# Kernel tuning notes

Hardware: AMD Instinct MI355X
Metric: run time of the kernel (lower is better)

Reference implementation:

```python
import jax, jax.numpy as jnp
import numpy as np

B, L, H = 16, 512, 1024
HEADS, HEAD_SIZE = 12, 64
NEG = 1e12


def sinusoidal_position_embedding(seq_len, output_dim):
    pos = jnp.arange(seq_len, dtype=jnp.float32)[:, None]
    idx = jnp.arange(output_dim // 2, dtype=jnp.float32)
    freqs = pos * jnp.power(10000.0, -2.0 * idx / output_dim)  # [L, D/2]
    emb = jnp.stack([jnp.sin(freqs), jnp.cos(freqs)], axis=-1)  # [L, D/2, 2]
    return emb.reshape(seq_len, output_dim)  # interleaved sin/cos, [L, D]


def setup_inputs() -> dict:
    key = jax.random.key(0)
    k1, k2, k3 = jax.random.split(key, 3)
    inputs = jax.random.normal(k1, (B, L, H), dtype=jnp.float32)
    mask = jnp.ones((B, L), dtype=jnp.int32)
    W = jax.random.normal(k2, (H, HEADS * HEAD_SIZE * 2), dtype=jnp.float32) / np.sqrt(H)
    b = jax.random.normal(k3, (HEADS * HEAD_SIZE * 2,), dtype=jnp.float32) * 0.01
    pos_emb = sinusoidal_position_embedding(L, HEAD_SIZE)  # [L, HEAD_SIZE]
    return {"inputs": inputs, "mask": mask, "W": W, "b": b, "pos_emb": pos_emb}


def rotate_half_interleaved(x):
    # stack([-x[..., 1::2], x[..., ::2]], -1).reshape(x.shape)
    x2 = jnp.stack([-x[..., 1::2], x[..., ::2]], axis=-1)
    return x2.reshape(x.shape)


def reference(inputs, mask, W, b, pos_emb):
    bsz, seq_len, _ = inputs.shape
    d = pos_emb.shape[-1]
    heads = W.shape[1] // (2 * d)
    out = inputs @ W + b                       # [B, L, heads*2d]
    out = out.reshape(bsz, seq_len, heads, 2 * d)
    qw, kw = out[..., :d], out[..., d:]        # [B, L, heads, d]
    cos_pos = jnp.repeat(pos_emb[:, 1::2], 2, axis=-1)[None, :, None, :]  # [1,L,1,d]
    sin_pos = jnp.repeat(pos_emb[:, 0::2], 2, axis=-1)[None, :, None, :]
    qw = qw * cos_pos + rotate_half_interleaved(qw) * sin_pos
    kw = kw * cos_pos + rotate_half_interleaved(kw) * sin_pos
    logits = jnp.einsum('bmhd,bnhd->bhmn', qw, kw)  # [B, heads, L, L]
    pad = mask.astype(logits.dtype)[:, None, None, :] * mask.astype(logits.dtype)[:, None, :, None]
    # torch code: expand of mask[:,None,None,:] -> applies along last axis only;
    # replicate exactly: pad_mask broadcasts mask over the query axis.
    pad_mask = jnp.broadcast_to(mask.astype(logits.dtype)[:, None, None, :], logits.shape)
    logits = logits * pad_mask - (1.0 - pad_mask) * NEG
    tril = jnp.tril(jnp.ones((seq_len, seq_len), dtype=logits.dtype), -1)
    logits = logits - tril[None, None, :, :] * NEG
    return logits / jnp.sqrt(jnp.array(d, dtype=logits.dtype))
```

## Files before the change

kernel.cpp:

```cpp
#include <hip/hip_runtime.h>

#define BB 16
#define LL 512
#define HH 1024
#define HEADS 12
#define DD 64
#define N1 1536
#define M1 8192
#define NEGC 1e12f

typedef short bf16x8 __attribute__((ext_vector_type(8)));
typedef float f32x4 __attribute__((ext_vector_type(4)));

__device__ __forceinline__ unsigned short f2bf(float f) {
    union { float f; unsigned int u; } v; v.f = f;
    unsigned int u = v.u;
    return (unsigned short)((u + 0x7fffu + ((u >> 16) & 1u)) >> 16);
}

__global__ __launch_bounds__(256) void k_conv_x(const float* __restrict__ X,
                                                unsigned short* __restrict__ Xb,
                                                int n4) {
    int i = blockIdx.x * 256 + threadIdx.x;
    if (i >= n4) return;
    float4 v = ((const float4*)X)[i];
    ushort4 o;
    o.x = f2bf(v.x); o.y = f2bf(v.y); o.z = f2bf(v.z); o.w = f2bf(v.w);
    ((ushort4*)Xb)[i] = o;
}

__global__ __launch_bounds__(256) void k_trans_w(const float* __restrict__ W,
                                                 unsigned short* __restrict__ Wt) {
    __shared__ float tile[32][33];
    int n0 = blockIdx.x * 32;
    int k0 = blockIdx.y * 32;
    int tx = threadIdx.x;
    int ty = threadIdx.y;
#pragma unroll
    for (int i = 0; i < 4; i++) {
        int k = ty + i * 8;
        tile[k][tx] = W[(size_t)(k0 + k) * N1 + n0 + tx];
    }
    __syncthreads();
#pragma unroll
    for (int i = 0; i < 4; i++) {
        int n = ty + i * 8;
        Wt[(size_t)(n0 + n) * HH + k0 + tx] = f2bf(tile[tx][n]);
    }
}

__global__ __launch_bounds__(256) void k_gemm1_rope(
    const unsigned short* __restrict__ Xb,
    const unsigned short* __restrict__ Wt,
    const float* __restrict__ bias,
    const float* __restrict__ pe,
    unsigned short* __restrict__ Qr,
    unsigned short* __restrict__ Kr)
{
    __shared__ __align__(16) unsigned short As[64 * 40];
    __shared__ __align__(16) unsigned short Bs[64 * 40];
    int m0 = blockIdx.y * 64;
    int n0 = blockIdx.x * 64;
    int tid = threadIdx.x;
    int w  = tid >> 6;
    int ln = tid & 63;
    int lq = ln >> 4;
    int lm = ln & 15;
    int mw = (w & 1) * 32;
    int nw = (w >> 1) * 32;

    int srow = tid >> 2;
    int scol = (tid & 3) * 8;

    f32x4 acc[2][2] = {};

    for (int kk = 0; kk < HH; kk += 32) {
        uint4 av = *(const uint4*)&Xb[(size_t)(m0 + srow) * HH + kk + scol];
        uint4 bv = *(const uint4*)&Wt[(size_t)(n0 + srow) * HH + kk + scol];
        *(uint4*)&As[srow * 40 + scol] = av;
        *(uint4*)&Bs[srow * 40 + scol] = bv;
        __syncthreads();
        bf16x8 af0 = *(const bf16x8*)&As[(mw + lm) * 40 + lq * 8];
        bf16x8 af1 = *(const bf16x8*)&As[(mw + 16 + lm) * 40 + lq * 8];
        bf16x8 bf0 = *(const bf16x8*)&Bs[(nw + lm) * 40 + lq * 8];
        bf16x8 bf1 = *(const bf16x8*)&Bs[(nw + 16 + lm) * 40 + lq * 8];
        acc[0][0] = __builtin_amdgcn_mfma_f32_16x16x32_bf16(af0, bf0, acc[0][0], 0, 0, 0);
        acc[0][1] = __builtin_amdgcn_mfma_f32_16x16x32_bf16(af0, bf1, acc[0][1], 0, 0, 0);
        acc[1][0] = __builtin_amdgcn_mfma_f32_16x16x32_bf16(af1, bf0, acc[1][0], 0, 0, 0);
        acc[1][1] = __builtin_amdgcn_mfma_f32_16x16x32_bf16(af1, bf1, acc[1][1], 0, 0, 0);
        __syncthreads();
    }

#pragma unroll
    for (int nt = 0; nt < 2; nt++) {
        int n = n0 + nw + nt * 16 + lm;
        float bv = bias[n];
        int h = n >> 7;
        int c = n & 127;
        int j = c & 63;
        int ii = j >> 1;
        bool isK = (c >= 64);
#pragma unroll
        for (int mt = 0; mt < 2; mt++) {
#pragma unroll
            for (int r = 0; r < 4; r++) {
                int m = m0 + mw + mt * 16 + lq * 4 + r;
                int l = m & (LL - 1);
                int bidx = m >> 9;
                float v = acc[mt][nt][r] + bv;
                float vp = __shfl_xor(v, 1, 64);
                float sv = pe[l * 64 + 2 * ii];
                float cv = pe[l * 64 + 2 * ii + 1];
                float o = (j & 1) ? (v * cv + vp * sv) : (v * cv - vp * sv);
                unsigned short ob = f2bf(o);
                size_t idx = ((size_t)(bidx * HEADS + h) * LL + l) * DD + j;
                if (isK) Kr[idx] = ob; else Qr[idx] = ob;
            }
        }
    }
}

__global__ __launch_bounds__(256) void k_gemm2(
    const unsigned short* __restrict__ Qr,
    const unsigned short* __restrict__ Kr,
    const int* __restrict__ mask,
    float* __restrict__ out)
{
    __shared__ __align__(16) unsigned short Qs[64 * 72];
    __shared__ __align__(16) unsigned short Ks[64 * 72];
    int bh = blockIdx.z;
    int b  = bh / HEADS;
    int n0 = blockIdx.x * 64;
    int m0 = blockIdx.y * 64;
    int tid = threadIdx.x;
    int w  = tid >> 6;
    int ln = tid & 63;
    int lq = ln >> 4;
    int lm = ln & 15;
    int mw = (w & 1) * 32;
    int nw = (w >> 1) * 32;

    const unsigned short* Qb = Qr + (size_t)bh * LL * DD;
    const unsigned short* Kb = Kr + (size_t)bh * LL * DD;

    int srow = tid >> 3;
    int scol = (tid & 7) * 8;
#pragma unroll
    for (int p = 0; p < 2; p++) {
        int row = srow + p * 32;
        *(uint4*)&Qs[row * 72 + scol] = *(const uint4*)&Qb[(size_t)(m0 + row) * DD + scol];
        *(uint4*)&Ks[row * 72 + scol] = *(const uint4*)&Kb[(size_t)(n0 + row) * DD + scol];
    }
    __syncthreads();

    f32x4 acc[2][2] = {};
#pragma unroll
    for (int kk = 0; kk < 64; kk += 32) {
        bf16x8 a0 = *(const bf16x8*)&Qs[(mw + lm) * 72 + kk + lq * 8];
        bf16x8 a1 = *(const bf16x8*)&Qs[(mw + 16 + lm) * 72 + kk + lq * 8];
        bf16x8 b0 = *(const bf16x8*)&Ks[(nw + lm) * 72 + kk + lq * 8];
        bf16x8 b1 = *(const bf16x8*)&Ks[(nw + 16 + lm) * 72 + kk + lq * 8];
        acc[0][0] = __builtin_amdgcn_mfma_f32_16x16x32_bf16(a0, b0, acc[0][0], 0, 0, 0);
        acc[0][1] = __builtin_amdgcn_mfma_f32_16x16x32_bf16(a0, b1, acc[0][1], 0, 0, 0);
        acc[1][0] = __builtin_amdgcn_mfma_f32_16x16x32_bf16(a1, b0, acc[1][0], 0, 0, 0);
        acc[1][1] = __builtin_amdgcn_mfma_f32_16x16x32_bf16(a1, b1, acc[1][1], 0, 0, 0);
    }

#pragma unroll
    for (int nt = 0; nt < 2; nt++) {
        int n = n0 + nw + nt * 16 + lm;
        float pm = (float)mask[b * LL + n];
        float negn = (1.0f - pm) * NEGC;
#pragma unroll
        for (int mt = 0; mt < 2; mt++) {
#pragma unroll
            for (int r = 0; r < 4; r++) {
                int m = m0 + mw + mt * 16 + lq * 4 + r;
                float dot = acc[mt][nt][r];
                float val = (dot * pm - negn - (n < m ? NEGC : 0.0f)) * 0.125f;
                out[((size_t)bh * LL + m) * LL + n] = val;
            }
        }
    }
}

extern "C" void kernel_launch(void* const* d_in, const int* in_sizes, int n_in,
                              void* d_out, int out_size, void* d_ws, size_t ws_size,
                              hipStream_t stream) {
    const float* X    = (const float*)d_in[0];
    const int*   mask = (const int*)d_in[1];
    const float* W    = (const float*)d_in[2];
    const float* bias = (const float*)d_in[3];
    const float* pe   = (const float*)d_in[4];
    float* out = (float*)d_out;

    char* ws = (char*)d_ws;
    unsigned short* Xb = (unsigned short*)ws;
    unsigned short* Wt = (unsigned short*)(ws + 16777216);
    unsigned short* Qr = (unsigned short*)(ws + 16777216 + 3145728);
    unsigned short* Kr = Qr + (size_t)BB * HEADS * LL * DD;

    k_conv_x<<<dim3((M1 * HH / 4 + 255) / 256), dim3(256), 0, stream>>>(X, Xb, M1 * HH / 4);
    k_trans_w<<<dim3(N1 / 32, HH / 32), dim3(32, 8), 0, stream>>>(W, Wt);
    k_gemm1_rope<<<dim3(N1 / 64, M1 / 64), dim3(256), 0, stream>>>(Xb, Wt, bias, pe, Qr, Kr);
    k_gemm2<<<dim3(LL / 64, LL / 64, BB * HEADS), dim3(256), 0, stream>>>(Qr, Kr, mask, out);
}
```

Before: 325.7 us.

## Enlarge GEMM1 tiles with direct global-to-LDS loads; vectorize GEMM2 output stores

GEMM1 tiles grow from 64x64 to 128x128, so each wave now owns a 64x64 sub-tile with 16 MFMAs per k-step. Operands are staged with global_load_lds, which copies straight into LDS without passing through registers, and the LDS row padding is removed. GEMM2 drops LDS staging and reads Q/K fragments directly from global memory. It swaps the MFMA operand order so each lane holds four consecutive output columns, which allows a vectorized 16-byte nontemporal store and a vectorized mask load. The unpadded LDS layout risks bank conflicts, and the larger tile means fewer blocks and higher register pressure.

```diff
diff --git a/kernel.cpp b/kernel.cpp
--- a/kernel.cpp
+++ b/kernel.cpp
@@ -12,10 +12,17 @@
 typedef short bf16x8 __attribute__((ext_vector_type(8)));
 typedef float f32x4 __attribute__((ext_vector_type(4)));
 
+typedef const __attribute__((address_space(1))) void* as1cvp;
+typedef __attribute__((address_space(3))) void* as3vp;
+
 __device__ __forceinline__ unsigned short f2bf(float f) {
     union { float f; unsigned int u; } v; v.f = f;
     unsigned int u = v.u;
     return (unsigned short)((u + 0x7fffu + ((u >> 16) & 1u)) >> 16);
+}
+
+__device__ __forceinline__ void gl_lds16(const void* g, void* l) {
+    __builtin_amdgcn_global_load_lds((as1cvp)g, (as3vp)l, 16, 0, 0);
 }
 
 __global__ __launch_bounds__(256) void k_conv_x(const float* __restrict__ X,
@@ -57,64 +64,74 @@
     unsigned short* __restrict__ Qr,
     unsigned short* __restrict__ Kr)
 {
-    __shared__ __align__(16) unsigned short As[64 * 40];
-    __shared__ __align__(16) unsigned short Bs[64 * 40];
-    int m0 = blockIdx.y * 64;
-    int n0 = blockIdx.x * 64;
+    __shared__ __align__(16) unsigned short As[128 * 32];
+    __shared__ __align__(16) unsigned short Bs[128 * 32];
+    int m0 = blockIdx.y * 128;
+    int n0 = blockIdx.x * 128;
     int tid = threadIdx.x;
     int w  = tid >> 6;
     int ln = tid & 63;
     int lq = ln >> 4;
     int lm = ln & 15;
-    int mw = (w & 1) * 32;
-    int nw = (w >> 1) * 32;
+    int wm = (w & 1) * 64;
+    int wn = (w >> 1) * 64;
 
     int srow = tid >> 2;
     int scol = (tid & 3) * 8;
-
-    f32x4 acc[2][2] = {};
+    const unsigned short* ga0 = &Xb[(size_t)(m0 + srow) * HH + scol];
+    const unsigned short* ga1 = &Xb[(size_t)(m0 + 64 + srow) * HH + scol];
+    const unsigned short* gb0 = &Wt[(size_t)(n0 + srow) * HH + scol];
+    const unsigned short* gb1 = &Wt[(size_t)(n0 + 64 + srow) * HH + scol];
+    unsigned short* la = &As[w * 512];
+    unsigned short* lb = &Bs[w * 512];
+
+    f32x4 acc[4][4] = {};
 
     for (int kk = 0; kk < HH; kk += 32) {
-        uint4 av = *(const uint4*)&Xb[(size_t)(m0 + srow) * HH + kk + scol];
-        uint4 bv = *(const uint4*)&Wt[(size_t)(n0 + srow) * HH + kk + scol];
-        *(uint4*)&As[srow * 40 + scol] = av;
-        *(uint4*)&Bs[srow * 40 + scol] = bv;
+        gl_lds16(ga0 + kk, la);
+        gl_lds16(ga1 + kk, la + 2048);
+        gl_lds16(gb0 + kk, lb);
+        gl_lds16(gb1 + kk, lb + 2048);
         __syncthreads();
-        bf16x8 af0 = *(const bf16x8*)&As[(mw + lm) * 40 + lq * 8];
-        bf16x8 af1 = *(const bf16x8*)&As[(mw + 16 + lm) * 40 + lq * 8];
-        bf16x8 bf0 = *(const bf16x8*)&Bs[(nw + lm) * 40 + lq * 8];
-        bf16x8 bf1 = *(const bf16x8*)&Bs[(nw + 16 + lm) * 40 + lq * 8];
-        acc[0][0] = __builtin_amdgcn_mfma_f32_16x16x32_bf16(af0, bf0, acc[0][0], 0, 0, 0);
-        acc[0][1] = __builtin_amdgcn_mfma_f32_16x16x32_bf16(af0, bf1, acc[0][1], 0, 0, 0);
-        acc[1][0] = __builtin_amdgcn_mfma_f32_16x16x32_bf16(af1, bf0, acc[1][0], 0, 0, 0);
-        acc[1][1] = __builtin_amdgcn_mfma_f32_16x16x32_bf16(af1, bf1, acc[1][1], 0, 0, 0);
+
+        bf16x8 a[4], b[4];
+#pragma unroll
+        for (int i = 0; i < 4; i++) {
+            a[i] = *(const bf16x8*)&As[(wm + i * 16 + lm) * 32 + lq * 8];
+            b[i] = *(const bf16x8*)&Bs[(wn + i * 16 + lm) * 32 + lq * 8];
+        }
+#pragma unroll
+        for (int mi = 0; mi < 4; mi++)
+#pragma unroll
+            for (int ni = 0; ni < 4; ni++)
+                acc[mi][ni] = __builtin_amdgcn_mfma_f32_16x16x32_bf16(
+                    a[mi], b[ni], acc[mi][ni], 0, 0, 0);
         __syncthreads();
     }
 
 #pragma unroll
-    for (int nt = 0; nt < 2; nt++) {
-        int n = n0 + nw + nt * 16 + lm;
+    for (int ni = 0; ni < 4; ni++) {
+        int n = n0 + wn + ni * 16 + lm;
         float bv = bias[n];
         int h = n >> 7;
         int c = n & 127;
         int j = c & 63;
         int ii = j >> 1;
         bool isK = (c >= 64);
-#pragma unroll
-        for (int mt = 0; mt < 2; mt++) {
+        unsigned short* dst = isK ? Kr : Qr;
+#pragma unroll
+        for (int mi = 0; mi < 4; mi++) {
 #pragma unroll
             for (int r = 0; r < 4; r++) {
-                int m = m0 + mw + mt * 16 + lq * 4 + r;
+                int m = m0 + wm + mi * 16 + lq * 4 + r;
                 int l = m & (LL - 1);
                 int bidx = m >> 9;
-                float v = acc[mt][nt][r] + bv;
+                float v = acc[mi][ni][r] + bv;
                 float vp = __shfl_xor(v, 1, 64);
-                float sv = pe[l * 64 + 2 * ii];
-                float cv = pe[l * 64 + 2 * ii + 1];
-                float o = (j & 1) ? (v * cv + vp * sv) : (v * cv - vp * sv);
-                unsigned short ob = f2bf(o);
+                float2 sc = *(const float2*)&pe[l * 64 + 2 * ii];
+                float o = (j & 1) ? (v * sc.y + vp * sc.x) : (v * sc.y - vp * sc.x);
                 size_t idx = ((size_t)(bidx * HEADS + h) * LL + l) * DD + j;
-                if (isK) Kr[idx] = ob; else Qr[idx] = ob;
+                dst[idx] = f2bf(o);
             }
         }
     }
@@ -126,8 +143,6 @@
     const int* __restrict__ mask,
     float* __restrict__ out)
 {
-    __shared__ __align__(16) unsigned short Qs[64 * 72];
-    __shared__ __align__(16) unsigned short Ks[64 * 72];
     int bh = blockIdx.z;
     int b  = bh / HEADS;
     int n0 = blockIdx.x * 64;
@@ -143,43 +158,36 @@
     const unsigned short* Qb = Qr + (size_t)bh * LL * DD;
     const unsigned short* Kb = Kr + (size_t)bh * LL * DD;
 
-    int srow = tid >> 3;
-    int scol = (tid & 7) * 8;
-#pragma unroll
-    for (int p = 0; p < 2; p++) {
-        int row = srow + p * 32;
-        *(uint4*)&Qs[row * 72 + scol] = *(const uint4*)&Qb[(size_t)(m0 + row) * DD + scol];
-        *(uint4*)&Ks[row * 72 + scol] = *(const uint4*)&Kb[(size_t)(n0 + row) * DD + scol];
-    }
-    __syncthreads();
-
     f32x4 acc[2][2] = {};
 #pragma unroll
     for (int kk = 0; kk < 64; kk += 32) {
-        bf16x8 a0 = *(const bf16x8*)&Qs[(mw + lm) * 72 + kk + lq * 8];
-        bf16x8 a1 = *(const bf16x8*)&Qs[(mw + 16 + lm) * 72 + kk + lq * 8];
-        bf16x8 b0 = *(const bf16x8*)&Ks[(nw + lm) * 72 + kk + lq * 8];
-        bf16x8 b1 = *(const bf16x8*)&Ks[(nw + 16 + lm) * 72 + kk + lq * 8];
-        acc[0][0] = __builtin_amdgcn_mfma_f32_16x16x32_bf16(a0, b0, acc[0][0], 0, 0, 0);
-        acc[0][1] = __builtin_amdgcn_mfma_f32_16x16x32_bf16(a0, b1, acc[0][1], 0, 0, 0);
-        acc[1][0] = __builtin_amdgcn_mfma_f32_16x16x32_bf16(a1, b0, acc[1][0], 0, 0, 0);
-        acc[1][1] = __builtin_amdgcn_mfma_f32_16x16x32_bf16(a1, b1, acc[1][1], 0, 0, 0);
+        bf16x8 q0 = *(const bf16x8*)&Qb[(size_t)(m0 + mw + lm) * DD + kk + lq * 8];
+        bf16x8 q1 = *(const bf16x8*)&Qb[(size_t)(m0 + mw + 16 + lm) * DD + kk + lq * 8];
+        bf16x8 k0 = *(const bf16x8*)&Kb[(size_t)(n0 + nw + lm) * DD + kk + lq * 8];
+        bf16x8 k1 = *(const bf16x8*)&Kb[(size_t)(n0 + nw + 16 + lm) * DD + kk + lq * 8];
+        acc[0][0] = __builtin_amdgcn_mfma_f32_16x16x32_bf16(k0, q0, acc[0][0], 0, 0, 0);
+        acc[0][1] = __builtin_amdgcn_mfma_f32_16x16x32_bf16(k0, q1, acc[0][1], 0, 0, 0);
+        acc[1][0] = __builtin_amdgcn_mfma_f32_16x16x32_bf16(k1, q0, acc[1][0], 0, 0, 0);
+        acc[1][1] = __builtin_amdgcn_mfma_f32_16x16x32_bf16(k1, q1, acc[1][1], 0, 0, 0);
     }
 
 #pragma unroll
     for (int nt = 0; nt < 2; nt++) {
-        int n = n0 + nw + nt * 16 + lm;
-        float pm = (float)mask[b * LL + n];
-        float negn = (1.0f - pm) * NEGC;
+        int nb = n0 + nw + nt * 16 + lq * 4;
+        int4 mv = *(const int4*)&mask[b * LL + nb];
 #pragma unroll
         for (int mt = 0; mt < 2; mt++) {
+            int m = m0 + mw + mt * 16 + lm;
+            f32x4 o;
 #pragma unroll
             for (int r = 0; r < 4; r++) {
-                int m = m0 + mw + mt * 16 + lq * 4 + r;
-                float dot = acc[mt][nt][r];
-                float val = (dot * pm - negn - (n < m ? NEGC : 0.0f)) * 0.125f;
-                out[((size_t)bh * LL + m) * LL + n] = val;
+                int n = nb + r;
+                float pm = (float)(((const int*)&mv)[r]);
+                float dot = acc[nt][mt][r];
+                float val = (dot * pm - (1.0f - pm) * NEGC - (n < m ? NEGC : 0.0f)) * 0.125f;
+                o[r] = val;
             }
+            __builtin_nontemporal_store(o, (f32x4*)&out[((size_t)bh * LL + m) * LL + nb]);
         }
     }
 }
@@ -202,6 +210,6 @@
 
     k_conv_x<<<dim3((M1 * HH / 4 + 255) / 256), dim3(256), 0, stream>>>(X, Xb, M1 * HH / 4);
     k_trans_w<<<dim3(N1 / 32, HH / 32), dim3(32, 8), 0, stream>>>(W, Wt);
-    k_gemm1_rope<<<dim3(N1 / 64, M1 / 64), dim3(256), 0, stream>>>(Xb, Wt, bias, pe, Qr, Kr);
+    k_gemm1_rope<<<dim3(N1 / 128, M1 / 128), dim3(256), 0, stream>>>(Xb, Wt, bias, pe, Qr, Kr);
     k_gemm2<<<dim3(LL / 64, LL / 64, BB * HEADS), dim3(256), 0, stream>>>(Qr, Kr, mask, out);
 }
```

Measured after the change: 322.3 us. Within noise of the previous version (-1.0%).
